# Optimization experiments

Hardware: AMD Instinct MI355X
Metric: run time of the kernel (lower is better)

## Reference

```python
import jax, jax.numpy as jnp
import numpy as np

ALPHA = 0.1
K = 10
N_NODES = 100000
N_EDGES = 3200000


def setup_inputs() -> dict:
    key = jax.random.key(0)
    ks = jax.random.split(key, 8)
    feat = jax.random.normal(ks[0], (N_NODES, 512), dtype=jnp.float32)
    W1 = jax.random.normal(ks[1], (512, 256), dtype=jnp.float32) * (1.0 / np.sqrt(512))
    b1 = jnp.zeros((256,), dtype=jnp.float32)
    W2 = jax.random.normal(ks[2], (256, 64), dtype=jnp.float32) * (1.0 / np.sqrt(256))
    b2 = jnp.zeros((64,), dtype=jnp.float32)
    edge_vals = jax.random.uniform(ks[3], (N_EDGES,), dtype=jnp.float32) / 32.0  # ~row-normalized
    edge_row = jax.random.randint(ks[4], (N_EDGES,), 0, N_NODES, dtype=jnp.int32)
    edge_col = jax.random.randint(ks[5], (N_EDGES,), 0, N_NODES, dtype=jnp.int32)
    return {"features": feat, "W1": W1, "b1": b1, "W2": W2, "b2": b2,
            "edge_vals": edge_vals, "edge_row": edge_row, "edge_col": edge_col}


def _spmm(edge_vals, edge_row, edge_col, x):
    # out[r] = sum_e vals[e] * x[col[e]]  for edges with row[e]==r
    msgs = edge_vals[:, None] * x[edge_col]  # [E, C]
    return jax.ops.segment_sum(msgs, edge_row, num_segments=N_NODES)


def reference(features, W1, b1, W2, b2, edge_vals, edge_row, edge_col):
    # MLP (dropout is identity in eval mode)
    x = jax.nn.relu(features @ W1 + b1)        # [N, nhid]
    x = x @ W2 + b2                             # [N, num_classes]
    h = x
    for _ in range(K):
        x = (1.0 - ALPHA) * _spmm(edge_vals, edge_row, edge_col, x) + ALPHA * h
    return jax.nn.log_softmax(x, axis=1)
```

## Files before the change

kernel.cpp:

```cpp
#include <hip/hip_runtime.h>
#include <hip/hip_bf16.h>
#include <math.h>

#define NNODES 100000
#define NFEAT 512
#define NHID 256
#define NCLS 64
#define ALPHA_C 0.1f

typedef short s16x8 __attribute__((ext_vector_type(8)));
typedef float f32x4 __attribute__((ext_vector_type(4)));

__device__ inline unsigned short f2b(float f) {
    union { float f; unsigned u; } v; v.f = f;
    unsigned r = v.u + 0x7fff + ((v.u >> 16) & 1);
    return (unsigned short)(r >> 16);
}
__device__ inline float b2f(unsigned short b) {
    return __uint_as_float((unsigned)b << 16);
}
__device__ inline float blo(unsigned u) { return __uint_as_float(u << 16); }
__device__ inline float bhi(unsigned u) { return __uint_as_float(u & 0xffff0000u); }

__global__ __launch_bounds__(256) void cvtT_kernel(
    const float* __restrict__ src, unsigned short* __restrict__ dst, int R, int Clog2)
{
    int idx = blockIdx.x * 256 + threadIdx.x;
    int C = 1 << Clog2;
    if (idx < R * C) {
        int r = idx >> Clog2, c = idx & (C - 1);
        dst[(size_t)c * R + r] = f2b(src[idx]);
    }
}

#define HID_STRIDE 264

__global__ __launch_bounds__(256) void mlp_mfma_kernel(
    const float* __restrict__ feat, const unsigned short* __restrict__ W1T,
    const float* __restrict__ b1, const unsigned short* __restrict__ W2T,
    const float* __restrict__ b2, unsigned short* __restrict__ h, int N)
{
    __shared__ unsigned short hid_s[64 * HID_STRIDE];
    const int tid  = threadIdx.x;
    const int w    = tid >> 6;
    const int lane = tid & 63;
    const int lr   = lane & 15;
    const int lh   = lane >> 4;
    const int m0   = blockIdx.x * 64;

    f32x4 acc[4][4];
#pragma unroll
    for (int i = 0; i < 4; ++i)
#pragma unroll
        for (int j = 0; j < 4; ++j) acc[i][j] = (f32x4)0.f;

    const float* arow[4];
#pragma unroll
    for (int mi = 0; mi < 4; ++mi) {
        int r = m0 + mi * 16 + lr;
        if (r > N - 1) r = N - 1;
        arow[mi] = feat + (size_t)r * NFEAT;
    }
    const unsigned short* brow[4];
#pragma unroll
    for (int nj = 0; nj < 4; ++nj)
        brow[nj] = W1T + (size_t)(w * 64 + nj * 16 + lr) * NFEAT;

    for (int kb = 0; kb < NFEAT; kb += 32) {
        const int k0 = kb + lh * 8;
        s16x8 afr[4], bfr[4];
#pragma unroll
        for (int mi = 0; mi < 4; ++mi) {
            float4 f0 = *reinterpret_cast<const float4*>(arow[mi] + k0);
            float4 f1 = *reinterpret_cast<const float4*>(arow[mi] + k0 + 4);
            s16x8 a;
            a[0] = f2b(f0.x); a[1] = f2b(f0.y); a[2] = f2b(f0.z); a[3] = f2b(f0.w);
            a[4] = f2b(f1.x); a[5] = f2b(f1.y); a[6] = f2b(f1.z); a[7] = f2b(f1.w);
            afr[mi] = a;
        }
#pragma unroll
        for (int nj = 0; nj < 4; ++nj)
            bfr[nj] = *reinterpret_cast<const s16x8*>(brow[nj] + k0);
#pragma unroll
        for (int mi = 0; mi < 4; ++mi)
#pragma unroll
            for (int nj = 0; nj < 4; ++nj)
                acc[mi][nj] = __builtin_amdgcn_mfma_f32_16x16x32_bf16(
                    afr[mi], bfr[nj], acc[mi][nj], 0, 0, 0);
    }

#pragma unroll
    for (int nj = 0; nj < 4; ++nj) {
        int col = w * 64 + nj * 16 + lr;
        float bias = b1[col];
#pragma unroll
        for (int mi = 0; mi < 4; ++mi)
#pragma unroll
            for (int q = 0; q < 4; ++q) {
                int row = mi * 16 + lh * 4 + q;
                hid_s[row * HID_STRIDE + col] = f2b(fmaxf(acc[mi][nj][q] + bias, 0.f));
            }
    }
    __syncthreads();

    f32x4 acc2[4];
#pragma unroll
    for (int i = 0; i < 4; ++i) acc2[i] = (f32x4)0.f;
    const int cw = w * 16;
    const unsigned short* b2row = W2T + (size_t)(cw + lr) * NHID;
    for (int ks = 0; ks < NHID; ks += 32) {
        int k0 = ks + lh * 8;
        s16x8 bfr = *reinterpret_cast<const s16x8*>(b2row + k0);
#pragma unroll
        for (int mi = 0; mi < 4; ++mi) {
            s16x8 afr = *reinterpret_cast<const s16x8*>(
                &hid_s[(mi * 16 + lr) * HID_STRIDE + k0]);
            acc2[mi] = __builtin_amdgcn_mfma_f32_16x16x32_bf16(afr, bfr, acc2[mi], 0, 0, 0);
        }
    }
    int col = cw + lr;
    float bias2 = b2[col];
#pragma unroll
    for (int mi = 0; mi < 4; ++mi)
#pragma unroll
        for (int q = 0; q < 4; ++q) {
            int row = m0 + mi * 16 + lh * 4 + q;
            if (row < N) h[(size_t)row * NCLS + col] = f2b(acc2[mi][q] + bias2);
        }
}

__global__ __launch_bounds__(256) void hist_kernel(
    const int* __restrict__ row, int* __restrict__ cnt, int E)
{
    int e = blockIdx.x * 256 + threadIdx.x;
    if (e < E) atomicAdd(&cnt[row[e]], 1);
}

__global__ __launch_bounds__(1024) void scan_kernel(
    int* __restrict__ cnt, int* __restrict__ row_ptr, int n)
{
    __shared__ int wsum[16];
    __shared__ int s_running;
    const int t = threadIdx.x, wid = t >> 6, lane = t & 63;
    if (t == 0) s_running = 0;
    __syncthreads();
    for (int base = 0; base < n; base += 1024) {
        int i = base + t;
        int c = (i < n) ? cnt[i] : 0;
        int x = c;
#pragma unroll
        for (int off = 1; off < 64; off <<= 1) {
            int y = __shfl_up(x, off);
            if (lane >= off) x += y;
        }
        if (lane == 63) wsum[wid] = x;
        __syncthreads();
        if (wid == 0 && lane < 16) {
            int wv = wsum[lane];
#pragma unroll
            for (int off = 1; off < 16; off <<= 1) {
                int y = __shfl_up(wv, off);
                if (lane >= off) wv += y;
            }
            wsum[lane] = wv;
        }
        __syncthreads();
        int woff = wid ? wsum[wid - 1] : 0;
        int incl = x + woff;
        int excl = incl - c;
        int run = s_running;
        if (i < n) { row_ptr[i] = run + excl; cnt[i] = run + excl; }
        __syncthreads();
        if (t == 1023) s_running = run + incl;
        __syncthreads();
    }
    if (t == 0) row_ptr[n] = s_running;
}

__global__ __launch_bounds__(256) void scatter_kernel(
    const float* __restrict__ vals, const int* __restrict__ row,
    const int* __restrict__ col, int* __restrict__ cursor,
    unsigned* __restrict__ ep, int E)
{
    int e = blockIdx.x * 256 + threadIdx.x;
    if (e < E) {
        int r = row[e];
        int pos = atomicAdd(&cursor[r], 1);
        unsigned q = (unsigned)__float2int_rn(vals[e] * 1048576.f);
        if (q > 32767u) q = 32767u;
        ep[pos] = ((unsigned)col[e] << 15) | q;
    }
}

__global__ __launch_bounds__(256) void spmm_kernel(
    const unsigned short* __restrict__ x_in, const unsigned short* __restrict__ h,
    unsigned short* __restrict__ x_out, const int* __restrict__ row_ptr,
    const unsigned* __restrict__ ep, int n)
{
    const int wid = threadIdx.x >> 6, lane = threadIdx.x & 63;
    const int r = blockIdx.x * 4 + wid;
    if (r >= n) return;
    const int g  = lane >> 4;
    const int li = lane & 15;
    const int s = row_ptr[r], e_end = row_ptr[r + 1];

    float aA0 = 0.f, aA1 = 0.f, aA2 = 0.f, aA3 = 0.f;
    float aB0 = 0.f, aB1 = 0.f, aB2 = 0.f, aB3 = 0.f;
    int e0 = s;
    for (; e0 + 8 <= e_end; e0 += 8) {
        unsigned p1 = ep[e0 + g];
        unsigned p2 = ep[e0 + 4 + g];
        int   c1 = (int)(p1 >> 15);
        float v1 = (float)(p1 & 0x7fffu) * (1.f / 1048576.f);
        int   c2 = (int)(p2 >> 15);
        float v2 = (float)(p2 & 0x7fffu) * (1.f / 1048576.f);
        uint2 u1 = *reinterpret_cast<const uint2*>(x_in + ((size_t)c1 << 6) + (li << 2));
        uint2 u2 = *reinterpret_cast<const uint2*>(x_in + ((size_t)c2 << 6) + (li << 2));
        aA0 += v1 * blo(u1.x); aA1 += v1 * bhi(u1.x);
        aA2 += v1 * blo(u1.y); aA3 += v1 * bhi(u1.y);
        aB0 += v2 * blo(u2.x); aB1 += v2 * bhi(u2.x);
        aB2 += v2 * blo(u2.y); aB3 += v2 * bhi(u2.y);
    }
    for (; e0 < e_end; e0 += 4) {
        int e = e0 + g;
        if (e < e_end) {
            unsigned p = ep[e];
            int   c = (int)(p >> 15);
            float v = (float)(p & 0x7fffu) * (1.f / 1048576.f);
            uint2 u = *reinterpret_cast<const uint2*>(x_in + ((size_t)c << 6) + (li << 2));
            aA0 += v * blo(u.x); aA1 += v * bhi(u.x);
            aA2 += v * blo(u.y); aA3 += v * bhi(u.y);
        }
    }
    float a0 = aA0 + aB0, a1 = aA1 + aB1, a2 = aA2 + aB2, a3 = aA3 + aB3;
#pragma unroll
    for (int off = 16; off < 64; off <<= 1) {
        a0 += __shfl_xor(a0, off);
        a1 += __shfl_xor(a1, off);
        a2 += __shfl_xor(a2, off);
        a3 += __shfl_xor(a3, off);
    }
    if (g == 0) {
        size_t o = ((size_t)r << 6) + (li << 2);
        uint2 hu = *reinterpret_cast<const uint2*>(h + o);
        float r0 = (1.f - ALPHA_C) * a0 + ALPHA_C * blo(hu.x);
        float r1 = (1.f - ALPHA_C) * a1 + ALPHA_C * bhi(hu.x);
        float r2 = (1.f - ALPHA_C) * a2 + ALPHA_C * blo(hu.y);
        float r3 = (1.f - ALPHA_C) * a3 + ALPHA_C * bhi(hu.y);
        uint2 ou;
        ou.x = ((unsigned)f2b(r1) << 16) | f2b(r0);
        ou.y = ((unsigned)f2b(r3) << 16) | f2b(r2);
        *reinterpret_cast<uint2*>(x_out + o) = ou;
    }
}

__global__ __launch_bounds__(256) void lsm_kernel(
    const unsigned short* __restrict__ x, float* __restrict__ out, int n)
{
    const int wid = threadIdx.x >> 6, lane = threadIdx.x & 63;
    const int r = blockIdx.x * 4 + wid;
    if (r >= n) return;
    float v = b2f(x[(size_t)r * NCLS + lane]);
    float m = v;
#pragma unroll
    for (int o = 32; o > 0; o >>= 1) m = fmaxf(m, __shfl_xor(m, o));
    float ex = expf(v - m);
    float s = ex;
#pragma unroll
    for (int o = 32; o > 0; o >>= 1) s += __shfl_xor(s, o);
    out[(size_t)r * NCLS + lane] = (v - m) - logf(s);
}

extern "C" void kernel_launch(void* const* d_in, const int* in_sizes, int n_in,
                              void* d_out, int out_size, void* d_ws, size_t ws_size,
                              hipStream_t stream)
{
    const float* feat = (const float*)d_in[0];
    const float* W1   = (const float*)d_in[1];
    const float* b1   = (const float*)d_in[2];
    const float* W2   = (const float*)d_in[3];
    const float* b2   = (const float*)d_in[4];
    const float* vals = (const float*)d_in[5];
    const int*   erow = (const int*)d_in[6];
    const int*   ecol = (const int*)d_in[7];
    const int N = in_sizes[0] / NFEAT;
    const int E = in_sizes[5];
    float* out = (float*)d_out;

    size_t off = 0;
    auto alloc = [&](size_t bytes) -> void* {
        void* p = (char*)d_ws + off;
        off += (bytes + 255) & ~(size_t)255;
        return p;
    };
    unsigned short* h       = (unsigned short*)alloc((size_t)N * NCLS * 2);
    unsigned short* xA      = (unsigned short*)alloc((size_t)N * NCLS * 2);
    unsigned short* xB      = (unsigned short*)alloc((size_t)N * NCLS * 2);
    int*            row_ptr = (int*)alloc((size_t)(N + 1) * 4);
    int*            cursor  = (int*)alloc((size_t)N * 4);
    unsigned*       ep      = (unsigned*)alloc((size_t)E * 4);
    unsigned short* W1T     = (unsigned short*)alloc((size_t)NHID * NFEAT * 2);
    unsigned short* W2T     = (unsigned short*)alloc((size_t)NCLS * NHID * 2);
    (void)ws_size;

    cvtT_kernel<<<(NFEAT * NHID + 255) / 256, 256, 0, stream>>>(W1, W1T, NFEAT, 8);
    cvtT_kernel<<<(NHID * NCLS + 255) / 256, 256, 0, stream>>>(W2, W2T, NHID, 6);

    mlp_mfma_kernel<<<(N + 63) / 64, 256, 0, stream>>>(feat, W1T, b1, W2T, b2, h, N);

    hipMemsetAsync(cursor, 0, (size_t)N * 4, stream);
    hist_kernel<<<(E + 255) / 256, 256, 0, stream>>>(erow, cursor, E);
    scan_kernel<<<1, 1024, 0, stream>>>(cursor, row_ptr, N);
    scatter_kernel<<<(E + 255) / 256, 256, 0, stream>>>(vals, erow, ecol, cursor, ep, E);

    const int gprop = (N + 3) / 4;
    const unsigned short* cur = h;
    for (int i = 0; i < 10; ++i) {
        unsigned short* dst = (i & 1) ? xB : xA;
        spmm_kernel<<<gprop, 256, 0, stream>>>(cur, h, dst, row_ptr, ep, N);
        cur = dst;
    }

    lsm_kernel<<<gprop, 256, 0, stream>>>(cur, out, N);
}
```

Before: 1.253 ms.

## Split node features into XCD-local column chunks and parallelize CSR scan

Stores the propagated node features as four 16-column chunks, each contiguous across all nodes. The SpMM block index is mapped so that each pair of XCDs handles one chunk, which shrinks the gather working set per XCD so it can stay in that die's L2 cache. Each wave now processes 8 edges at a time with narrower 4-byte loads, and the MLP output and log-softmax are updated for the new layout. The single-block serial prefix scan is replaced with a three-kernel block-parallel scan. The trade-off is that each edge index is now read four times, once per chunk, and there are more blocks and more scan launches.

```diff
diff --git a/kernel.cpp b/kernel.cpp
--- a/kernel.cpp
+++ b/kernel.cpp
@@ -120,12 +120,13 @@
     }
     int col = cw + lr;
     float bias2 = b2[col];
+    const size_t cbase = (size_t)(col >> 4) * N * 16 + (col & 15);
 #pragma unroll
     for (int mi = 0; mi < 4; ++mi)
 #pragma unroll
         for (int q = 0; q < 4; ++q) {
             int row = m0 + mi * 16 + lh * 4 + q;
-            if (row < N) h[(size_t)row * NCLS + col] = f2b(acc2[mi][q] + bias2);
+            if (row < N) h[cbase + (size_t)row * 16] = f2b(acc2[mi][q] + bias2);
         }
 }
 
@@ -136,45 +137,65 @@
     if (e < E) atomicAdd(&cnt[row[e]], 1);
 }
 
-__global__ __launch_bounds__(1024) void scan_kernel(
-    int* __restrict__ cnt, int* __restrict__ row_ptr, int n)
+__global__ __launch_bounds__(1024) void scanA_kernel(
+    const int* __restrict__ cnt, int* __restrict__ excl, int* __restrict__ partials, int n)
 {
     __shared__ int wsum[16];
-    __shared__ int s_running;
     const int t = threadIdx.x, wid = t >> 6, lane = t & 63;
-    if (t == 0) s_running = 0;
+    const int i = blockIdx.x * 1024 + t;
+    int c = (i < n) ? cnt[i] : 0;
+    int x = c;
+#pragma unroll
+    for (int off = 1; off < 64; off <<= 1) {
+        int y = __shfl_up(x, off);
+        if (lane >= off) x += y;
+    }
+    if (lane == 63) wsum[wid] = x;
     __syncthreads();
-    for (int base = 0; base < n; base += 1024) {
-        int i = base + t;
-        int c = (i < n) ? cnt[i] : 0;
-        int x = c;
-#pragma unroll
-        for (int off = 1; off < 64; off <<= 1) {
-            int y = __shfl_up(x, off);
-            if (lane >= off) x += y;
-        }
-        if (lane == 63) wsum[wid] = x;
+    if (wid == 0 && lane < 16) {
+        int wv = wsum[lane];
+#pragma unroll
+        for (int off = 1; off < 16; off <<= 1) {
+            int y = __shfl_up(wv, off);
+            if (lane >= off) wv += y;
+        }
+        wsum[lane] = wv;
+    }
+    __syncthreads();
+    int woff = wid ? wsum[wid - 1] : 0;
+    int incl = x + woff;
+    if (i < n) excl[i] = incl - c;
+    if (t == 1023) partials[blockIdx.x] = incl;
+}
+
+__global__ __launch_bounds__(256) void scanB_kernel(
+    int* __restrict__ partials, int* __restrict__ row_ptr_end, int nb, int n)
+{
+    __shared__ int s[256];
+    const int t = threadIdx.x;
+    int v = (t < nb) ? partials[t] : 0;
+    s[t] = v;
+    __syncthreads();
+    for (int off = 1; off < 256; off <<= 1) {
+        int y = (t >= off) ? s[t - off] : 0;
         __syncthreads();
-        if (wid == 0 && lane < 16) {
-            int wv = wsum[lane];
-#pragma unroll
-            for (int off = 1; off < 16; off <<= 1) {
-                int y = __shfl_up(wv, off);
-                if (lane >= off) wv += y;
-            }
-            wsum[lane] = wv;
-        }
+        s[t] += y;
         __syncthreads();
-        int woff = wid ? wsum[wid - 1] : 0;
-        int incl = x + woff;
-        int excl = incl - c;
-        int run = s_running;
-        if (i < n) { row_ptr[i] = run + excl; cnt[i] = run + excl; }
-        __syncthreads();
-        if (t == 1023) s_running = run + incl;
-        __syncthreads();
-    }
-    if (t == 0) row_ptr[n] = s_running;
+    }
+    partials[t] = s[t] - v;
+    if (t == 255) row_ptr_end[n] = s[255];
+}
+
+__global__ __launch_bounds__(1024) void scanC_kernel(
+    int* __restrict__ row_ptr, int* __restrict__ cursor,
+    const int* __restrict__ partials, int n)
+{
+    const int i = blockIdx.x * 1024 + threadIdx.x;
+    if (i < n) {
+        int v = row_ptr[i] + partials[blockIdx.x];
+        row_ptr[i] = v;
+        cursor[i] = v;
+    }
 }
 
 __global__ __launch_bounds__(256) void scatter_kernel(
@@ -195,62 +216,57 @@
 __global__ __launch_bounds__(256) void spmm_kernel(
     const unsigned short* __restrict__ x_in, const unsigned short* __restrict__ h,
     unsigned short* __restrict__ x_out, const int* __restrict__ row_ptr,
-    const unsigned* __restrict__ ep, int n)
-{
+    const unsigned* __restrict__ ep, int n, int G)
+{
+    const int b = blockIdx.x;
+    const int xcd = b & 7;
+    const int chunk = xcd >> 1;
+    const int rg = (b >> 3) * 2 + (xcd & 1);
+    if (rg >= G) return;
     const int wid = threadIdx.x >> 6, lane = threadIdx.x & 63;
-    const int r = blockIdx.x * 4 + wid;
+    const int r = rg * 4 + wid;
     if (r >= n) return;
-    const int g  = lane >> 4;
-    const int li = lane & 15;
+    const int g  = lane >> 3;
+    const int li = lane & 7;
+    const unsigned short* xc = x_in + (size_t)chunk * n * 16;
     const int s = row_ptr[r], e_end = row_ptr[r + 1];
 
-    float aA0 = 0.f, aA1 = 0.f, aA2 = 0.f, aA3 = 0.f;
-    float aB0 = 0.f, aB1 = 0.f, aB2 = 0.f, aB3 = 0.f;
+    float aA0 = 0.f, aA1 = 0.f, aB0 = 0.f, aB1 = 0.f;
     int e0 = s;
-    for (; e0 + 8 <= e_end; e0 += 8) {
+    for (; e0 + 16 <= e_end; e0 += 16) {
         unsigned p1 = ep[e0 + g];
-        unsigned p2 = ep[e0 + 4 + g];
+        unsigned p2 = ep[e0 + 8 + g];
         int   c1 = (int)(p1 >> 15);
         float v1 = (float)(p1 & 0x7fffu) * (1.f / 1048576.f);
         int   c2 = (int)(p2 >> 15);
         float v2 = (float)(p2 & 0x7fffu) * (1.f / 1048576.f);
-        uint2 u1 = *reinterpret_cast<const uint2*>(x_in + ((size_t)c1 << 6) + (li << 2));
-        uint2 u2 = *reinterpret_cast<const uint2*>(x_in + ((size_t)c2 << 6) + (li << 2));
-        aA0 += v1 * blo(u1.x); aA1 += v1 * bhi(u1.x);
-        aA2 += v1 * blo(u1.y); aA3 += v1 * bhi(u1.y);
-        aB0 += v2 * blo(u2.x); aB1 += v2 * bhi(u2.x);
-        aB2 += v2 * blo(u2.y); aB3 += v2 * bhi(u2.y);
-    }
-    for (; e0 < e_end; e0 += 4) {
+        unsigned u1 = *reinterpret_cast<const unsigned*>(xc + ((size_t)c1 << 4) + (li << 1));
+        unsigned u2 = *reinterpret_cast<const unsigned*>(xc + ((size_t)c2 << 4) + (li << 1));
+        aA0 += v1 * blo(u1); aA1 += v1 * bhi(u1);
+        aB0 += v2 * blo(u2); aB1 += v2 * bhi(u2);
+    }
+    for (; e0 < e_end; e0 += 8) {
         int e = e0 + g;
         if (e < e_end) {
             unsigned p = ep[e];
             int   c = (int)(p >> 15);
             float v = (float)(p & 0x7fffu) * (1.f / 1048576.f);
-            uint2 u = *reinterpret_cast<const uint2*>(x_in + ((size_t)c << 6) + (li << 2));
-            aA0 += v * blo(u.x); aA1 += v * bhi(u.x);
-            aA2 += v * blo(u.y); aA3 += v * bhi(u.y);
-        }
-    }
-    float a0 = aA0 + aB0, a1 = aA1 + aB1, a2 = aA2 + aB2, a3 = aA3 + aB3;
-#pragma unroll
-    for (int off = 16; off < 64; off <<= 1) {
+            unsigned u = *reinterpret_cast<const unsigned*>(xc + ((size_t)c << 4) + (li << 1));
+            aA0 += v * blo(u); aA1 += v * bhi(u);
+        }
+    }
+    float a0 = aA0 + aB0, a1 = aA1 + aB1;
+#pragma unroll
+    for (int off = 8; off < 64; off <<= 1) {
         a0 += __shfl_xor(a0, off);
         a1 += __shfl_xor(a1, off);
-        a2 += __shfl_xor(a2, off);
-        a3 += __shfl_xor(a3, off);
     }
     if (g == 0) {
-        size_t o = ((size_t)r << 6) + (li << 2);
-        uint2 hu = *reinterpret_cast<const uint2*>(h + o);
-        float r0 = (1.f - ALPHA_C) * a0 + ALPHA_C * blo(hu.x);
-        float r1 = (1.f - ALPHA_C) * a1 + ALPHA_C * bhi(hu.x);
-        float r2 = (1.f - ALPHA_C) * a2 + ALPHA_C * blo(hu.y);
-        float r3 = (1.f - ALPHA_C) * a3 + ALPHA_C * bhi(hu.y);
-        uint2 ou;
-        ou.x = ((unsigned)f2b(r1) << 16) | f2b(r0);
-        ou.y = ((unsigned)f2b(r3) << 16) | f2b(r2);
-        *reinterpret_cast<uint2*>(x_out + o) = ou;
+        size_t o = (size_t)chunk * n * 16 + ((size_t)r << 4) + (li << 1);
+        unsigned hu = *reinterpret_cast<const unsigned*>(h + o);
+        float r0 = (1.f - ALPHA_C) * a0 + ALPHA_C * blo(hu);
+        float r1 = (1.f - ALPHA_C) * a1 + ALPHA_C * bhi(hu);
+        *reinterpret_cast<unsigned*>(x_out + o) = ((unsigned)f2b(r1) << 16) | f2b(r0);
     }
 }
 
@@ -260,7 +276,7 @@
     const int wid = threadIdx.x >> 6, lane = threadIdx.x & 63;
     const int r = blockIdx.x * 4 + wid;
     if (r >= n) return;
-    float v = b2f(x[(size_t)r * NCLS + lane]);
+    float v = b2f(x[(size_t)(lane >> 4) * n * 16 + (size_t)r * 16 + (lane & 15)]);
     float m = v;
 #pragma unroll
     for (int o = 32; o > 0; o >>= 1) m = fmaxf(m, __shfl_xor(m, o));
@@ -293,14 +309,16 @@
         off += (bytes + 255) & ~(size_t)255;
         return p;
     };
-    unsigned short* h       = (unsigned short*)alloc((size_t)N * NCLS * 2);
-    unsigned short* xA      = (unsigned short*)alloc((size_t)N * NCLS * 2);
-    unsigned short* xB      = (unsigned short*)alloc((size_t)N * NCLS * 2);
-    int*            row_ptr = (int*)alloc((size_t)(N + 1) * 4);
-    int*            cursor  = (int*)alloc((size_t)N * 4);
-    unsigned*       ep      = (unsigned*)alloc((size_t)E * 4);
-    unsigned short* W1T     = (unsigned short*)alloc((size_t)NHID * NFEAT * 2);
-    unsigned short* W2T     = (unsigned short*)alloc((size_t)NCLS * NHID * 2);
+    unsigned short* h        = (unsigned short*)alloc((size_t)N * NCLS * 2);
+    unsigned short* xA       = (unsigned short*)alloc((size_t)N * NCLS * 2);
+    unsigned short* xB       = (unsigned short*)alloc((size_t)N * NCLS * 2);
+    int*            row_ptr  = (int*)alloc((size_t)(N + 1) * 4);
+    int*            cnt      = (int*)alloc((size_t)N * 4);
+    int*            cursor   = (int*)alloc((size_t)N * 4);
+    int*            partials = (int*)alloc(256 * 4);
+    unsigned*       ep       = (unsigned*)alloc((size_t)E * 4);
+    unsigned short* W1T      = (unsigned short*)alloc((size_t)NHID * NFEAT * 2);
+    unsigned short* W2T      = (unsigned short*)alloc((size_t)NCLS * NHID * 2);
     (void)ws_size;
 
     cvtT_kernel<<<(NFEAT * NHID + 255) / 256, 256, 0, stream>>>(W1, W1T, NFEAT, 8);
@@ -308,18 +326,22 @@
 
     mlp_mfma_kernel<<<(N + 63) / 64, 256, 0, stream>>>(feat, W1T, b1, W2T, b2, h, N);
 
-    hipMemsetAsync(cursor, 0, (size_t)N * 4, stream);
-    hist_kernel<<<(E + 255) / 256, 256, 0, stream>>>(erow, cursor, E);
-    scan_kernel<<<1, 1024, 0, stream>>>(cursor, row_ptr, N);
+    hipMemsetAsync(cnt, 0, (size_t)N * 4, stream);
+    hist_kernel<<<(E + 255) / 256, 256, 0, stream>>>(erow, cnt, E);
+    const int nb = (N + 1023) / 1024;
+    scanA_kernel<<<nb, 1024, 0, stream>>>(cnt, row_ptr, partials, N);
+    scanB_kernel<<<1, 256, 0, stream>>>(partials, row_ptr, nb, N);
+    scanC_kernel<<<nb, 1024, 0, stream>>>(row_ptr, cursor, partials, N);
     scatter_kernel<<<(E + 255) / 256, 256, 0, stream>>>(vals, erow, ecol, cursor, ep, E);
 
-    const int gprop = (N + 3) / 4;
+    const int G = (N + 3) / 4;
+    const int gprop = 8 * ((G + 1) / 2);
     const unsigned short* cur = h;
     for (int i = 0; i < 10; ++i) {
         unsigned short* dst = (i & 1) ? xB : xA;
-        spmm_kernel<<<gprop, 256, 0, stream>>>(cur, h, dst, row_ptr, ep, N);
+        spmm_kernel<<<gprop, 256, 0, stream>>>(cur, h, dst, row_ptr, ep, N, G);
         cur = dst;
     }
 
-    lsm_kernel<<<gprop, 256, 0, stream>>>(cur, out, N);
-}
+    lsm_kernel<<<(N + 3) / 4, 256, 0, stream>>>(cur, out, N);
+}
```

Result: slower. 1.914 ms (+52.7%).

## Parallelize CSR scan and use two-level bucketed scatter for edge sort

Applied to the files above, without the earlier changes.

Replaces the single-block sequential prefix scan with a three-kernel multi-block scan (block scan, partials scan, add-back). Replaces the per-row atomic scatter with a two-pass bucketed scatter: edges are first binned into 4096 row buckets through a global atomic cursor per bucket, then each bucket is placed row by row using shared-memory atomics. The aim is to cut the serial scan latency and make the random scatter writes more local. The cost is an extra 8-byte-per-edge staging buffer and additional passes over the edges. Bucket-level global atomics are also more contended.

```diff
diff --git a/kernel.cpp b/kernel.cpp
--- a/kernel.cpp
+++ b/kernel.cpp
@@ -7,6 +7,7 @@
 #define NHID 256
 #define NCLS 64
 #define ALPHA_C 0.1f
+#define NB 4096
 
 typedef short s16x8 __attribute__((ext_vector_type(8)));
 typedef float f32x4 __attribute__((ext_vector_type(4)));
@@ -136,59 +137,106 @@
     if (e < E) atomicAdd(&cnt[row[e]], 1);
 }
 
-__global__ __launch_bounds__(1024) void scan_kernel(
-    int* __restrict__ cnt, int* __restrict__ row_ptr, int n)
+__global__ __launch_bounds__(1024) void scanA_kernel(
+    const int* __restrict__ cnt, int* __restrict__ excl, int* __restrict__ partials, int n)
 {
     __shared__ int wsum[16];
-    __shared__ int s_running;
     const int t = threadIdx.x, wid = t >> 6, lane = t & 63;
-    if (t == 0) s_running = 0;
-    __syncthreads();
-    for (int base = 0; base < n; base += 1024) {
-        int i = base + t;
-        int c = (i < n) ? cnt[i] : 0;
-        int x = c;
-#pragma unroll
-        for (int off = 1; off < 64; off <<= 1) {
-            int y = __shfl_up(x, off);
-            if (lane >= off) x += y;
-        }
-        if (lane == 63) wsum[wid] = x;
+    const int i = blockIdx.x * 1024 + t;
+    int c = (i < n) ? cnt[i] : 0;
+    int x = c;
+#pragma unroll
+    for (int off = 1; off < 64; off <<= 1) {
+        int y = __shfl_up(x, off);
+        if (lane >= off) x += y;
+    }
+    if (lane == 63) wsum[wid] = x;
+    __syncthreads();
+    if (wid == 0 && lane < 16) {
+        int wv = wsum[lane];
+#pragma unroll
+        for (int off = 1; off < 16; off <<= 1) {
+            int y = __shfl_up(wv, off);
+            if (lane >= off) wv += y;
+        }
+        wsum[lane] = wv;
+    }
+    __syncthreads();
+    int woff = wid ? wsum[wid - 1] : 0;
+    int incl = x + woff;
+    if (i < n) excl[i] = incl - c;
+    if (t == 1023) partials[blockIdx.x] = incl;
+}
+
+__global__ __launch_bounds__(256) void scanB_kernel(
+    int* __restrict__ partials, int* __restrict__ row_ptr_end, int nb, int n)
+{
+    __shared__ int s[256];
+    const int t = threadIdx.x;
+    int v = (t < nb) ? partials[t] : 0;
+    s[t] = v;
+    __syncthreads();
+    for (int off = 1; off < 256; off <<= 1) {
+        int y = (t >= off) ? s[t - off] : 0;
         __syncthreads();
-        if (wid == 0 && lane < 16) {
-            int wv = wsum[lane];
-#pragma unroll
-            for (int off = 1; off < 16; off <<= 1) {
-                int y = __shfl_up(wv, off);
-                if (lane >= off) wv += y;
-            }
-            wsum[lane] = wv;
-        }
+        s[t] += y;
         __syncthreads();
-        int woff = wid ? wsum[wid - 1] : 0;
-        int incl = x + woff;
-        int excl = incl - c;
-        int run = s_running;
-        if (i < n) { row_ptr[i] = run + excl; cnt[i] = run + excl; }
-        __syncthreads();
-        if (t == 1023) s_running = run + incl;
-        __syncthreads();
-    }
-    if (t == 0) row_ptr[n] = s_running;
-}
-
-__global__ __launch_bounds__(256) void scatter_kernel(
+    }
+    partials[t] = s[t] - v;
+    if (t == 255) row_ptr_end[n] = s[255];
+}
+
+__global__ __launch_bounds__(1024) void scanC_kernel(
+    int* __restrict__ row_ptr, const int* __restrict__ partials, int n)
+{
+    const int i = blockIdx.x * 1024 + threadIdx.x;
+    if (i < n) row_ptr[i] += partials[blockIdx.x];
+}
+
+__global__ __launch_bounds__(256) void binit_kernel(
+    const int* __restrict__ row_ptr, int* __restrict__ bcur, int RB, int n)
+{
+    int b = blockIdx.x * 256 + threadIdx.x;
+    if (b < NB) {
+        int r = b * RB; if (r > n) r = n;
+        bcur[b] = row_ptr[r];
+    }
+}
+
+__global__ __launch_bounds__(256) void scatterA_kernel(
     const float* __restrict__ vals, const int* __restrict__ row,
-    const int* __restrict__ col, int* __restrict__ cursor,
-    unsigned* __restrict__ ep, int E)
+    const int* __restrict__ col, int* __restrict__ bcur,
+    unsigned long long* __restrict__ stage, int E, int RB)
 {
     int e = blockIdx.x * 256 + threadIdx.x;
     if (e < E) {
         int r = row[e];
-        int pos = atomicAdd(&cursor[r], 1);
+        int b = r / RB;
         unsigned q = (unsigned)__float2int_rn(vals[e] * 1048576.f);
         if (q > 32767u) q = 32767u;
-        ep[pos] = ((unsigned)col[e] << 15) | q;
+        unsigned lo = ((unsigned)col[e] << 15) | q;
+        int pos = atomicAdd(&bcur[b], 1);
+        stage[pos] = ((unsigned long long)(unsigned)r << 32) | lo;
+    }
+}
+
+__global__ __launch_bounds__(256) void scatterB_kernel(
+    const unsigned long long* __restrict__ stage, const int* __restrict__ row_ptr,
+    unsigned* __restrict__ ep, int RB, int n)
+{
+    __shared__ int lcur[64];
+    const int b = blockIdx.x;
+    const int r0 = b * RB;
+    if (r0 >= n) return;
+    const int r1 = min(r0 + RB, n);
+    const int s0 = row_ptr[r0], s1 = row_ptr[r1];
+    for (int i = threadIdx.x; i < r1 - r0; i += 256) lcur[i] = row_ptr[r0 + i];
+    __syncthreads();
+    for (int i = s0 + threadIdx.x; i < s1; i += 256) {
+        unsigned long long rec = stage[i];
+        int r = (int)(rec >> 32);
+        int p = atomicAdd(&lcur[r - r0], 1);
+        ep[p] = (unsigned)rec;
     }
 }
 
@@ -286,6 +334,7 @@
     const int N = in_sizes[0] / NFEAT;
     const int E = in_sizes[5];
     float* out = (float*)d_out;
+    const int RB = (N + NB - 1) / NB;
 
     size_t off = 0;
     auto alloc = [&](size_t bytes) -> void* {
@@ -293,14 +342,17 @@
         off += (bytes + 255) & ~(size_t)255;
         return p;
     };
-    unsigned short* h       = (unsigned short*)alloc((size_t)N * NCLS * 2);
-    unsigned short* xA      = (unsigned short*)alloc((size_t)N * NCLS * 2);
-    unsigned short* xB      = (unsigned short*)alloc((size_t)N * NCLS * 2);
-    int*            row_ptr = (int*)alloc((size_t)(N + 1) * 4);
-    int*            cursor  = (int*)alloc((size_t)N * 4);
-    unsigned*       ep      = (unsigned*)alloc((size_t)E * 4);
-    unsigned short* W1T     = (unsigned short*)alloc((size_t)NHID * NFEAT * 2);
-    unsigned short* W2T     = (unsigned short*)alloc((size_t)NCLS * NHID * 2);
+    unsigned short*     h        = (unsigned short*)alloc((size_t)N * NCLS * 2);
+    unsigned short*     xA       = (unsigned short*)alloc((size_t)N * NCLS * 2);
+    unsigned short*     xB       = (unsigned short*)alloc((size_t)N * NCLS * 2);
+    int*                row_ptr  = (int*)alloc((size_t)(N + 1) * 4);
+    int*                cnt      = (int*)alloc((size_t)N * 4);
+    int*                partials = (int*)alloc(256 * 4);
+    int*                bcur     = (int*)alloc((size_t)NB * 4);
+    unsigned*           ep       = (unsigned*)alloc((size_t)E * 4);
+    unsigned long long* stage    = (unsigned long long*)alloc((size_t)E * 8);
+    unsigned short*     W1T      = (unsigned short*)alloc((size_t)NHID * NFEAT * 2);
+    unsigned short*     W2T      = (unsigned short*)alloc((size_t)NCLS * NHID * 2);
     (void)ws_size;
 
     cvtT_kernel<<<(NFEAT * NHID + 255) / 256, 256, 0, stream>>>(W1, W1T, NFEAT, 8);
@@ -308,10 +360,15 @@
 
     mlp_mfma_kernel<<<(N + 63) / 64, 256, 0, stream>>>(feat, W1T, b1, W2T, b2, h, N);
 
-    hipMemsetAsync(cursor, 0, (size_t)N * 4, stream);
-    hist_kernel<<<(E + 255) / 256, 256, 0, stream>>>(erow, cursor, E);
-    scan_kernel<<<1, 1024, 0, stream>>>(cursor, row_ptr, N);
-    scatter_kernel<<<(E + 255) / 256, 256, 0, stream>>>(vals, erow, ecol, cursor, ep, E);
+    hipMemsetAsync(cnt, 0, (size_t)N * 4, stream);
+    hist_kernel<<<(E + 255) / 256, 256, 0, stream>>>(erow, cnt, E);
+    const int nb = (N + 1023) / 1024;
+    scanA_kernel<<<nb, 1024, 0, stream>>>(cnt, row_ptr, partials, N);
+    scanB_kernel<<<1, 256, 0, stream>>>(partials, row_ptr, nb, N);
+    scanC_kernel<<<nb, 1024, 0, stream>>>(row_ptr, partials, N);
+    binit_kernel<<<NB / 256, 256, 0, stream>>>(row_ptr, bcur, RB, N);
+    scatterA_kernel<<<(E + 255) / 256, 256, 0, stream>>>(vals, erow, ecol, bcur, stage, E, RB);
+    scatterB_kernel<<<NB, 256, 0, stream>>>(stage, row_ptr, ep, RB, N);
 
     const int gprop = (N + 3) / 4;
     const unsigned short* cur = h;
@@ -321,5 +378,5 @@
         cur = dst;
     }
 
-    lsm_kernel<<<gprop, 256, 0, stream>>>(cur, out, N);
-}
+    lsm_kernel<<<(N + 3) / 4, 256, 0, stream>>>(cur, out, N);
+}
```

Result: no change. 1.257 ms (+0.3%).

## Partition CSR edges by column chunk for cache-local SpMM gathers

Applied to the files above, without the earlier changes.

Replaces the per-row CSR build with a two-level counting sort keyed by column chunk (16K nodes) and row bucket, producing a per-chunk row pointer array. The SpMM kernel now processes 49-row blocks, iterating over column chunks so gathered x rows stay within a cache-sized window, accumulating partial sums in shared memory. This is meant to improve L2 locality of the random gathers, at the cost of a heavier preprocessing pipeline (staging buffer, multiple scans) and lower per-row parallelism in SpMM.

```diff
diff --git a/kernel.cpp b/kernel.cpp
--- a/kernel.cpp
+++ b/kernel.cpp
@@ -7,6 +7,13 @@
 #define NHID 256
 #define NCLS 64
 #define ALPHA_C 0.1f
+
+#define CHUNK_SHIFT 14
+#define NBUCKET 128
+#define RB2 782
+#define NPB 256
+#define KMAX 1024
+#define ROWS_PB 49
 
 typedef short s16x8 __attribute__((ext_vector_type(8)));
 typedef float f32x4 __attribute__((ext_vector_type(4)));
@@ -129,127 +136,207 @@
         }
 }
 
-__global__ __launch_bounds__(256) void hist_kernel(
-    const int* __restrict__ row, int* __restrict__ cnt, int E)
-{
-    int e = blockIdx.x * 256 + threadIdx.x;
-    if (e < E) atomicAdd(&cnt[row[e]], 1);
-}
-
-__global__ __launch_bounds__(1024) void scan_kernel(
-    int* __restrict__ cnt, int* __restrict__ row_ptr, int n)
+
+__global__ __launch_bounds__(256) void countP1_kernel(
+    const int* __restrict__ erow, const int* __restrict__ ecol,
+    int* __restrict__ cnt_t, int E, int CE, int K)
+{
+    __shared__ int c[KMAX];
+    const int blk = blockIdx.x, t = threadIdx.x;
+    for (int i = t; i < K; i += 256) c[i] = 0;
+    __syncthreads();
+    const int e0 = blk * CE, e1 = min(e0 + CE, E);
+    for (int e = e0 + t; e < e1; e += 256) {
+        int key = (ecol[e] >> CHUNK_SHIFT) * NBUCKET + erow[e] / RB2;
+        atomicAdd(&c[key], 1);
+    }
+    __syncthreads();
+    for (int k = t; k < K; k += 256)
+        cnt_t[(size_t)blk * K + k] = c[k];
+}
+
+__global__ __launch_bounds__(256) void keytot_kernel(
+    const int* __restrict__ cnt_t, int* __restrict__ keytot, int K)
+{
+    int k = blockIdx.x * 256 + threadIdx.x;
+    if (k < K) {
+        int s = 0;
+        for (int b = 0; b < NPB; ++b) s += cnt_t[(size_t)b * K + k];
+        keytot[k] = s;
+    }
+}
+
+__global__ __launch_bounds__(1024) void keyscan_kernel(
+    const int* __restrict__ keytot, int* __restrict__ keybase, int K)
 {
     __shared__ int wsum[16];
-    __shared__ int s_running;
     const int t = threadIdx.x, wid = t >> 6, lane = t & 63;
-    if (t == 0) s_running = 0;
-    __syncthreads();
-    for (int base = 0; base < n; base += 1024) {
-        int i = base + t;
-        int c = (i < n) ? cnt[i] : 0;
-        int x = c;
-#pragma unroll
-        for (int off = 1; off < 64; off <<= 1) {
-            int y = __shfl_up(x, off);
-            if (lane >= off) x += y;
+    int c = (t < K) ? keytot[t] : 0;
+    int x = c;
+#pragma unroll
+    for (int off = 1; off < 64; off <<= 1) {
+        int y = __shfl_up(x, off);
+        if (lane >= off) x += y;
+    }
+    if (lane == 63) wsum[wid] = x;
+    __syncthreads();
+    if (wid == 0 && lane < 16) {
+        int wv = wsum[lane];
+#pragma unroll
+        for (int off = 1; off < 16; off <<= 1) {
+            int y = __shfl_up(wv, off);
+            if (lane >= off) wv += y;
         }
-        if (lane == 63) wsum[wid] = x;
-        __syncthreads();
-        if (wid == 0 && lane < 16) {
-            int wv = wsum[lane];
-#pragma unroll
-            for (int off = 1; off < 16; off <<= 1) {
-                int y = __shfl_up(wv, off);
-                if (lane >= off) wv += y;
-            }
-            wsum[lane] = wv;
-        }
-        __syncthreads();
-        int woff = wid ? wsum[wid - 1] : 0;
-        int incl = x + woff;
-        int excl = incl - c;
-        int run = s_running;
-        if (i < n) { row_ptr[i] = run + excl; cnt[i] = run + excl; }
-        __syncthreads();
-        if (t == 1023) s_running = run + incl;
-        __syncthreads();
-    }
-    if (t == 0) row_ptr[n] = s_running;
-}
-
-__global__ __launch_bounds__(256) void scatter_kernel(
-    const float* __restrict__ vals, const int* __restrict__ row,
-    const int* __restrict__ col, int* __restrict__ cursor,
-    unsigned* __restrict__ ep, int E)
-{
-    int e = blockIdx.x * 256 + threadIdx.x;
-    if (e < E) {
-        int r = row[e];
-        int pos = atomicAdd(&cursor[r], 1);
+        wsum[lane] = wv;
+    }
+    __syncthreads();
+    int woff = wid ? wsum[wid - 1] : 0;
+    int incl = x + woff;
+    if (t < K) keybase[t] = incl - c;
+    if (t == 1023) keybase[K] = wsum[15];
+}
+
+__global__ __launch_bounds__(256) void colscan_kernel(
+    const int* __restrict__ cnt_t, const int* __restrict__ keybase,
+    int* __restrict__ Sblk, int K)
+{
+    int k = blockIdx.x * 256 + threadIdx.x;
+    if (k >= K) return;
+    int run = keybase[k];
+    for (int b = 0; b < NPB; ++b) {
+        size_t idx = (size_t)b * K + k;
+        int v = cnt_t[idx];
+        Sblk[idx] = run;
+        run += v;
+    }
+}
+
+__global__ __launch_bounds__(256) void scatterA_kernel(
+    const float* __restrict__ vals, const int* __restrict__ erow,
+    const int* __restrict__ ecol, const int* __restrict__ Sblk,
+    unsigned long long* __restrict__ stage, int E, int CE, int K)
+{
+    __shared__ int lcur[KMAX];
+    const int blk = blockIdx.x, t = threadIdx.x;
+    for (int k = t; k < K; k += 256) lcur[k] = Sblk[(size_t)blk * K + k];
+    __syncthreads();
+    const int e0 = blk * CE, e1 = min(e0 + CE, E);
+    for (int e = e0 + t; e < e1; e += 256) {
+        int r = erow[e], cc = ecol[e];
         unsigned q = (unsigned)__float2int_rn(vals[e] * 1048576.f);
         if (q > 32767u) q = 32767u;
-        ep[pos] = ((unsigned)col[e] << 15) | q;
+        unsigned lo = ((unsigned)cc << 15) | q;
+        int key = (cc >> CHUNK_SHIFT) * NBUCKET + r / RB2;
+        int pos = atomicAdd(&lcur[key], 1);
+        stage[pos] = ((unsigned long long)(unsigned)r << 32) | lo;
+    }
+}
+
+__global__ __launch_bounds__(1024) void scatterB_kernel(
+    const unsigned long long* __restrict__ stage, const int* __restrict__ keybase,
+    unsigned* __restrict__ ep, int* __restrict__ rp2, int n, int nchunk)
+{
+    __shared__ int hcnt[1024];
+    __shared__ int hscan[1024];
+    const int k = blockIdx.x, t = threadIdx.x;
+    if (k == 0 && t == 0) rp2[(size_t)nchunk * n] = keybase[NBUCKET * nchunk];
+    const int j   = k >> 7;
+    const int bkt = k & (NBUCKET - 1);
+    const int r0  = bkt * RB2;
+    if (r0 >= n) return;
+    const int nr = min(RB2, n - r0);
+    const int s0 = keybase[k], s1 = keybase[k + 1];
+    hcnt[t] = 0;
+    __syncthreads();
+    for (int i = s0 + t; i < s1; i += 1024)
+        atomicAdd(&hcnt[(int)(stage[i] >> 32) - r0], 1);
+    __syncthreads();
+    int v = hcnt[t];
+    hscan[t] = v;
+    __syncthreads();
+    for (int off = 1; off < 1024; off <<= 1) {
+        int y = (t >= off) ? hscan[t - off] : 0;
+        __syncthreads();
+        hscan[t] += y;
+        __syncthreads();
+    }
+    int excl = hscan[t] - v;
+    if (t < nr) rp2[(size_t)j * n + r0 + t] = s0 + excl;
+    __syncthreads();
+    hscan[t] = s0 + excl;
+    __syncthreads();
+    for (int i = s0 + t; i < s1; i += 1024) {
+        unsigned long long rec = stage[i];
+        int p = atomicAdd(&hscan[(int)(rec >> 32) - r0], 1);
+        ep[p] = (unsigned)rec;
     }
 }
 
 __global__ __launch_bounds__(256) void spmm_kernel(
     const unsigned short* __restrict__ x_in, const unsigned short* __restrict__ h,
-    unsigned short* __restrict__ x_out, const int* __restrict__ row_ptr,
-    const unsigned* __restrict__ ep, int n)
-{
-    const int wid = threadIdx.x >> 6, lane = threadIdx.x & 63;
-    const int r = blockIdx.x * 4 + wid;
-    if (r >= n) return;
-    const int g  = lane >> 4;
+    unsigned short* __restrict__ x_out, const int* __restrict__ rp2,
+    const unsigned* __restrict__ ep, int n, int nchunk)
+{
+    __shared__ float acc[ROWS_PB * 64];
+    const int r0 = blockIdx.x * ROWS_PB;
+    if (r0 >= n) return;
+    const int nr = min(ROWS_PB, n - r0);
+    const int t = threadIdx.x;
+    const int lane = t & 63;
+    const int gg = (t >> 6) * 4 + (lane >> 4);
     const int li = lane & 15;
-    const int s = row_ptr[r], e_end = row_ptr[r + 1];
-
-    float aA0 = 0.f, aA1 = 0.f, aA2 = 0.f, aA3 = 0.f;
-    float aB0 = 0.f, aB1 = 0.f, aB2 = 0.f, aB3 = 0.f;
-    int e0 = s;
-    for (; e0 + 8 <= e_end; e0 += 8) {
-        unsigned p1 = ep[e0 + g];
-        unsigned p2 = ep[e0 + 4 + g];
-        int   c1 = (int)(p1 >> 15);
-        float v1 = (float)(p1 & 0x7fffu) * (1.f / 1048576.f);
-        int   c2 = (int)(p2 >> 15);
-        float v2 = (float)(p2 & 0x7fffu) * (1.f / 1048576.f);
-        uint2 u1 = *reinterpret_cast<const uint2*>(x_in + ((size_t)c1 << 6) + (li << 2));
-        uint2 u2 = *reinterpret_cast<const uint2*>(x_in + ((size_t)c2 << 6) + (li << 2));
-        aA0 += v1 * blo(u1.x); aA1 += v1 * bhi(u1.x);
-        aA2 += v1 * blo(u1.y); aA3 += v1 * bhi(u1.y);
-        aB0 += v2 * blo(u2.x); aB1 += v2 * bhi(u2.x);
-        aB2 += v2 * blo(u2.y); aB3 += v2 * bhi(u2.y);
-    }
-    for (; e0 < e_end; e0 += 4) {
-        int e = e0 + g;
-        if (e < e_end) {
-            unsigned p = ep[e];
-            int   c = (int)(p >> 15);
-            float v = (float)(p & 0x7fffu) * (1.f / 1048576.f);
-            uint2 u = *reinterpret_cast<const uint2*>(x_in + ((size_t)c << 6) + (li << 2));
-            aA0 += v * blo(u.x); aA1 += v * bhi(u.x);
-            aA2 += v * blo(u.y); aA3 += v * bhi(u.y);
+
+    for (int i = t; i < nr * 64; i += 256) acc[i] = 0.f;
+    __syncthreads();
+
+    for (int j = 0; j < nchunk; ++j) {
+        const int* rpj = rp2 + (size_t)j * n;
+        for (int lr = gg; lr < nr; lr += 16) {
+            int r = r0 + lr;
+            int s = rpj[r], e = rpj[r + 1];
+            float a0 = 0.f, a1 = 0.f, a2 = 0.f, a3 = 0.f;
+            int e0 = s;
+            for (; e0 + 2 <= e; e0 += 2) {
+                unsigned p1 = ep[e0];
+                unsigned p2 = ep[e0 + 1];
+                int   c1 = (int)(p1 >> 15);
+                int   c2 = (int)(p2 >> 15);
+                float v1 = (float)(p1 & 0x7fffu) * (1.f / 1048576.f);
+                float v2 = (float)(p2 & 0x7fffu) * (1.f / 1048576.f);
+                uint2 u1 = *reinterpret_cast<const uint2*>(x_in + ((size_t)c1 << 6) + (li << 2));
+                uint2 u2 = *reinterpret_cast<const uint2*>(x_in + ((size_t)c2 << 6) + (li << 2));
+                a0 += v1 * blo(u1.x); a1 += v1 * bhi(u1.x);
+                a2 += v1 * blo(u1.y); a3 += v1 * bhi(u1.y);
+                a0 += v2 * blo(u2.x); a1 += v2 * bhi(u2.x);
+                a2 += v2 * blo(u2.y); a3 += v2 * bhi(u2.y);
+            }
+            if (e0 < e) {
+                unsigned p = ep[e0];
+                int   c = (int)(p >> 15);
+                float v = (float)(p & 0x7fffu) * (1.f / 1048576.f);
+                uint2 u = *reinterpret_cast<const uint2*>(x_in + ((size_t)c << 6) + (li << 2));
+                a0 += v * blo(u.x); a1 += v * bhi(u.x);
+                a2 += v * blo(u.y); a3 += v * bhi(u.y);
+            }
+            float* ap = &acc[lr * 64 + li * 4];
+            ap[0] += a0; ap[1] += a1; ap[2] += a2; ap[3] += a3;
         }
     }
-    float a0 = aA0 + aB0, a1 = aA1 + aB1, a2 = aA2 + aB2, a3 = aA3 + aB3;
-#pragma unroll
-    for (int off = 16; off < 64; off <<= 1) {
-        a0 += __shfl_xor(a0, off);
-        a1 += __shfl_xor(a1, off);
-        a2 += __shfl_xor(a2, off);
-        a3 += __shfl_xor(a3, off);
-    }
-    if (g == 0) {
-        size_t o = ((size_t)r << 6) + (li << 2);
-        uint2 hu = *reinterpret_cast<const uint2*>(h + o);
-        float r0 = (1.f - ALPHA_C) * a0 + ALPHA_C * blo(hu.x);
-        float r1 = (1.f - ALPHA_C) * a1 + ALPHA_C * bhi(hu.x);
-        float r2 = (1.f - ALPHA_C) * a2 + ALPHA_C * blo(hu.y);
-        float r3 = (1.f - ALPHA_C) * a3 + ALPHA_C * bhi(hu.y);
+    __syncthreads();
+
+    for (int i = t; i < nr * 16; i += 256) {
+        int lr = i >> 4, q = i & 15;
+        const float* ap = &acc[lr * 64 + q * 4];
+        size_t o = ((size_t)(r0 + lr) << 6) + (q << 2);
+        const unsigned* hp = reinterpret_cast<const unsigned*>(h + o);
+        unsigned hx = hp[0], hy = hp[1];
+        float r0f = (1.f - ALPHA_C) * ap[0] + ALPHA_C * blo(hx);
+        float r1f = (1.f - ALPHA_C) * ap[1] + ALPHA_C * bhi(hx);
+        float r2f = (1.f - ALPHA_C) * ap[2] + ALPHA_C * blo(hy);
+        float r3f = (1.f - ALPHA_C) * ap[3] + ALPHA_C * bhi(hy);
         uint2 ou;
-        ou.x = ((unsigned)f2b(r1) << 16) | f2b(r0);
-        ou.y = ((unsigned)f2b(r3) << 16) | f2b(r2);
+        ou.x = ((unsigned)f2b(r1f) << 16) | f2b(r0f);
+        ou.y = ((unsigned)f2b(r3f) << 16) | f2b(r2f);
         *reinterpret_cast<uint2*>(x_out + o) = ou;
     }
 }
@@ -286,6 +373,10 @@
     const int N = in_sizes[0] / NFEAT;
     const int E = in_sizes[5];
     float* out = (float*)d_out;
+    const int NCHUNK = (N + (1 << CHUNK_SHIFT) - 1) >> CHUNK_SHIFT;
+    const int K  = NCHUNK * NBUCKET;
+    const int CE = (E + NPB - 1) / NPB;
+    const int NC = K * NPB;
 
     size_t off = 0;
     auto alloc = [&](size_t bytes) -> void* {
@@ -293,14 +384,18 @@
         off += (bytes + 255) & ~(size_t)255;
         return p;
     };
-    unsigned short* h       = (unsigned short*)alloc((size_t)N * NCLS * 2);
-    unsigned short* xA      = (unsigned short*)alloc((size_t)N * NCLS * 2);
-    unsigned short* xB      = (unsigned short*)alloc((size_t)N * NCLS * 2);
-    int*            row_ptr = (int*)alloc((size_t)(N + 1) * 4);
-    int*            cursor  = (int*)alloc((size_t)N * 4);
-    unsigned*       ep      = (unsigned*)alloc((size_t)E * 4);
-    unsigned short* W1T     = (unsigned short*)alloc((size_t)NHID * NFEAT * 2);
-    unsigned short* W2T     = (unsigned short*)alloc((size_t)NCLS * NHID * 2);
+    unsigned short*     h       = (unsigned short*)alloc((size_t)N * NCLS * 2);
+    unsigned short*     xA      = (unsigned short*)alloc((size_t)N * NCLS * 2);
+    unsigned short*     xB      = (unsigned short*)alloc((size_t)N * NCLS * 2);
+    int*                rp2     = (int*)alloc(((size_t)NCHUNK * N + 1) * 4);
+    int*                cnt_t   = (int*)alloc((size_t)NC * 4);
+    int*                Sblk    = (int*)alloc((size_t)NC * 4);
+    int*                keytot  = (int*)alloc((size_t)K * 4);
+    int*                keybase = (int*)alloc((size_t)(K + 1) * 4);
+    unsigned*           ep      = (unsigned*)alloc((size_t)E * 4);
+    unsigned long long* stage   = (unsigned long long*)alloc((size_t)E * 8);
+    unsigned short*     W1T     = (unsigned short*)alloc((size_t)NHID * NFEAT * 2);
+    unsigned short*     W2T     = (unsigned short*)alloc((size_t)NCLS * NHID * 2);
     (void)ws_size;
 
     cvtT_kernel<<<(NFEAT * NHID + 255) / 256, 256, 0, stream>>>(W1, W1T, NFEAT, 8);
@@ -308,18 +403,20 @@
 
     mlp_mfma_kernel<<<(N + 63) / 64, 256, 0, stream>>>(feat, W1T, b1, W2T, b2, h, N);
 
-    hipMemsetAsync(cursor, 0, (size_t)N * 4, stream);
-    hist_kernel<<<(E + 255) / 256, 256, 0, stream>>>(erow, cursor, E);
-    scan_kernel<<<1, 1024, 0, stream>>>(cursor, row_ptr, N);
-    scatter_kernel<<<(E + 255) / 256, 256, 0, stream>>>(vals, erow, ecol, cursor, ep, E);
-
-    const int gprop = (N + 3) / 4;
+    countP1_kernel<<<NPB, 256, 0, stream>>>(erow, ecol, cnt_t, E, CE, K);
+    keytot_kernel<<<(K + 255) / 256, 256, 0, stream>>>(cnt_t, keytot, K);
+    keyscan_kernel<<<1, 1024, 0, stream>>>(keytot, keybase, K);
+    colscan_kernel<<<(K + 255) / 256, 256, 0, stream>>>(cnt_t, keybase, Sblk, K);
+    scatterA_kernel<<<NPB, 256, 0, stream>>>(vals, erow, ecol, Sblk, stage, E, CE, K);
+    scatterB_kernel<<<K, 1024, 0, stream>>>(stage, keybase, ep, rp2, N, NCHUNK);
+
+    const int gprop = (N + ROWS_PB - 1) / ROWS_PB;
     const unsigned short* cur = h;
     for (int i = 0; i < 10; ++i) {
         unsigned short* dst = (i & 1) ? xB : xA;
-        spmm_kernel<<<gprop, 256, 0, stream>>>(cur, h, dst, row_ptr, ep, N);
+        spmm_kernel<<<gprop, 256, 0, stream>>>(cur, h, dst, rp2, ep, N, NCHUNK);
         cur = dst;
     }
 
-    lsm_kernel<<<gprop, 256, 0, stream>>>(cur, out, N);
-}
+    lsm_kernel<<<(N + 3) / 4, 256, 0, stream>>>(cur, out, N);
+}
```

Measured after the change: 1.183 ms. 1.06x faster.
